# Optimization experiments

Hardware: AMD Instinct MI355X
Metric: run time of the kernel (lower is better)

The kernel has to match this reference:

```python
import jax, jax.numpy as jnp
import numpy as np

D_MODEL = 1024
N_HEADS = 16
D_K = D_MODEL // N_HEADS  # 64


def setup_inputs() -> dict:
    key = jax.random.key(0)
    ks = jax.random.split(key, 12)
    B, S = 2, 2048
    inp = {
        "query": jax.random.normal(ks[0], (B, S, D_MODEL), jnp.float32),
        "key": jax.random.normal(ks[1], (B, S, D_MODEL), jnp.float32),
        "value": jax.random.normal(ks[2], (B, S, D_MODEL), jnp.float32),
        "mask": jnp.ones((B, 1, S, S), jnp.int32),
    }
    sc = 1.0 / np.sqrt(D_MODEL)
    inp["Wq"] = jax.random.normal(ks[3], (D_MODEL, D_MODEL), jnp.float32) * sc
    inp["bq"] = jnp.zeros((D_MODEL,), jnp.float32)
    inp["Wk"] = jax.random.normal(ks[4], (D_MODEL, D_MODEL), jnp.float32) * sc
    inp["bk"] = jnp.zeros((D_MODEL,), jnp.float32)
    inp["Wv"] = jax.random.normal(ks[5], (D_MODEL, D_MODEL), jnp.float32) * sc
    inp["bv"] = jnp.zeros((D_MODEL,), jnp.float32)
    inp["Wo"] = jax.random.normal(ks[6], (D_MODEL, D_MODEL), jnp.float32) * sc
    inp["bo"] = jnp.zeros((D_MODEL,), jnp.float32)
    return inp


def reference(query, key, value, mask, Wq, bq, Wk, bk, Wv, bv, Wo, bo):
    B, Sq, _ = query.shape
    H, dk = N_HEADS, D_K
    # linear projections, split heads: (B,S,D) -> (B,H,S,dk)
    def split_heads(x):
        return x.reshape(B, -1, H, dk).transpose(0, 2, 1, 3)
    Q = split_heads(query @ Wq.T + bq)
    K = split_heads(key @ Wk.T + bk)
    V = split_heads(value @ Wv.T + bv)
    scale = 1.0 / jnp.sqrt(jnp.asarray(dk, jnp.float32))
    scores = jnp.einsum('bhqd,bhkd->bhqk', Q, K) * scale
    scores = jnp.where(mask == 0, jnp.asarray(-1e9, scores.dtype), scores)
    attn = jax.nn.softmax(scores, axis=-1)  # (B,H,Sq,Sk)
    out = jnp.einsum('bhqk,bhkd->bhqd', attn, V)
    out = out.transpose(0, 2, 1, 3).reshape(B, Sq, D_MODEL)
    out = out @ Wo.T + bo
    return out, attn
```

## Files before the change

### kernel.cpp

```cpp
#include <hip/hip_runtime.h>
#include <cstdint>
#include <cstddef>

#define DEV __device__ __forceinline__

typedef float f32x4 __attribute__((ext_vector_type(4)));
typedef __bf16 bf16x8 __attribute__((ext_vector_type(8)));
typedef unsigned short u16x8 __attribute__((ext_vector_type(8)));

static constexpr int D = 1024, H = 16, DK = 64, S = 2048, B = 2;
static constexpr int M_TOT = B * S;
static constexpr size_t OUT0 = (size_t)M_TOT * D;

DEV unsigned short f2bf(float f) {
  unsigned x = __builtin_bit_cast(unsigned, f);
  unsigned r = (x + 0x7fffu + ((x >> 16) & 1u)) >> 16;
  return (unsigned short)r;
}

DEV float bf2f(unsigned short u) {
  return __builtin_bit_cast(float, (unsigned)u << 16);
}

DEV f32x4 mfma_bf16(bf16x8 a, bf16x8 b, f32x4 c) {
  return __builtin_amdgcn_mfma_f32_16x16x32_bf16(a, b, c, 0, 0, 0);
}

DEV bf16x8 bc(u16x8 u) { return __builtin_bit_cast(bf16x8, u); }

template <int MODE, bool ABF16>
DEV void proj_body(unsigned short* As, unsigned short* Bs, const void* Aptr,
                   const unsigned short* W, const float* bias, void* dst) {
  constexpr int BM = 128, BK = 32, LDT = 40;
  const int tid = threadIdx.x;
  const int lane = tid & 63, wave = tid >> 6;
  const int wrow = wave >> 1, wcol = wave & 1;
  const int l15 = lane & 15, kg = lane >> 4;
  const int m0 = blockIdx.y * BM, n0 = blockIdx.x * BM;
  const int srow = tid >> 1, scb = (tid & 1) * 16;

  f32x4 acc[4][4] = {};

  for (int kt = 0; kt < D; kt += BK) {
    {
      u16x8 t0, t1;
      if constexpr (ABF16) {
        const unsigned short* ap =
            (const unsigned short*)Aptr + (size_t)(m0 + srow) * D + kt + scb;
        t0 = *(const u16x8*)ap;
        t1 = *(const u16x8*)(ap + 8);
      } else {
        const float* ap = (const float*)Aptr + (size_t)(m0 + srow) * D + kt + scb;
        float4 v0 = *(const float4*)(ap + 0);
        float4 v1 = *(const float4*)(ap + 4);
        float4 v2 = *(const float4*)(ap + 8);
        float4 v3 = *(const float4*)(ap + 12);
        t0[0] = f2bf(v0.x); t0[1] = f2bf(v0.y); t0[2] = f2bf(v0.z); t0[3] = f2bf(v0.w);
        t0[4] = f2bf(v1.x); t0[5] = f2bf(v1.y); t0[6] = f2bf(v1.z); t0[7] = f2bf(v1.w);
        t1[0] = f2bf(v2.x); t1[1] = f2bf(v2.y); t1[2] = f2bf(v2.z); t1[3] = f2bf(v2.w);
        t1[4] = f2bf(v3.x); t1[5] = f2bf(v3.y); t1[6] = f2bf(v3.z); t1[7] = f2bf(v3.w);
      }
      *(u16x8*)&As[srow * LDT + scb] = t0;
      *(u16x8*)&As[srow * LDT + scb + 8] = t1;

      const unsigned short* wp = W + (size_t)(n0 + srow) * D + kt + scb;
      *(u16x8*)&Bs[srow * LDT + scb] = *(const u16x8*)wp;
      *(u16x8*)&Bs[srow * LDT + scb + 8] = *(const u16x8*)(wp + 8);
    }
    __syncthreads();

    bf16x8 a[4], b[4];
#pragma unroll
    for (int i = 0; i < 4; i++)
      a[i] = bc(*(const u16x8*)&As[(wrow * 64 + i * 16 + l15) * LDT + kg * 8]);
#pragma unroll
    for (int i = 0; i < 4; i++)
      b[i] = bc(*(const u16x8*)&Bs[(wcol * 64 + i * 16 + l15) * LDT + kg * 8]);
#pragma unroll
    for (int mi = 0; mi < 4; mi++)
#pragma unroll
      for (int ni = 0; ni < 4; ni++) acc[mi][ni] = mfma_bf16(a[mi], b[ni], acc[mi][ni]);
    __syncthreads();
  }

#pragma unroll
  for (int mi = 0; mi < 4; mi++) {
#pragma unroll
    for (int ni = 0; ni < 4; ni++) {
      const int n = n0 + wcol * 64 + ni * 16 + l15;
      const float bval = bias[n];
#pragma unroll
      for (int r = 0; r < 4; r++) {
        const int m = m0 + wrow * 64 + mi * 16 + kg * 4 + r;
        float v = acc[mi][ni][r] + bval;
        if constexpr (MODE == 0) v *= 0.125f;
        if constexpr (MODE == 0 || MODE == 1) {
          const int b_ = m >> 11, s = m & (S - 1), h = n >> 6, d_ = n & (DK - 1);
          ((unsigned short*)dst)[(((size_t)(b_ * H + h)) * S + s) * DK + d_] = f2bf(v);
        } else if constexpr (MODE == 2) {
          const int b_ = m >> 11, s = m & (S - 1), h = n >> 6, d_ = n & (DK - 1);
          ((unsigned short*)dst)[(((size_t)(b_ * H + h)) * DK + d_) * S + s] = f2bf(v);
        } else {
          ((float*)dst)[(size_t)m * D + n] = v;
        }
      }
    }
  }
}

__global__ __launch_bounds__(256) void conv_kernel(
    const float* __restrict__ Wq, const float* __restrict__ Wk,
    const float* __restrict__ Wv, const float* __restrict__ Wo,
    unsigned short* __restrict__ Wqb, unsigned short* __restrict__ Wkb,
    unsigned short* __restrict__ Wvb, unsigned short* __restrict__ Wob,
    const int* __restrict__ mask, unsigned long long* __restrict__ bits) {
  const int gid = blockIdx.x, tid = threadIdx.x;
  if (gid < 256) {
    const float* srcs[4] = {Wq, Wk, Wv, Wo};
    unsigned short* dsts[4] = {Wqb, Wkb, Wvb, Wob};
    const float* src = srcs[gid >> 6];
    unsigned short* dst = dsts[gid >> 6];
    const size_t off = (size_t)(gid & 63) * 16384;
#pragma unroll
    for (int it = 0; it < 4; it++) {
      const size_t i0 = off + it * 4096 + (size_t)tid * 16;
      float4 v0 = *(const float4*)(src + i0);
      float4 v1 = *(const float4*)(src + i0 + 4);
      float4 v2 = *(const float4*)(src + i0 + 8);
      float4 v3 = *(const float4*)(src + i0 + 12);
      u16x8 t0, t1;
      t0[0] = f2bf(v0.x); t0[1] = f2bf(v0.y); t0[2] = f2bf(v0.z); t0[3] = f2bf(v0.w);
      t0[4] = f2bf(v1.x); t0[5] = f2bf(v1.y); t0[6] = f2bf(v1.z); t0[7] = f2bf(v1.w);
      t1[0] = f2bf(v2.x); t1[1] = f2bf(v2.y); t1[2] = f2bf(v2.z); t1[3] = f2bf(v2.w);
      t1[4] = f2bf(v3.x); t1[5] = f2bf(v3.y); t1[6] = f2bf(v3.z); t1[7] = f2bf(v3.w);
      *(u16x8*)(dst + i0) = t0;
      *(u16x8*)(dst + i0 + 8) = t1;
    }
  } else {
    const int lane = tid & 63;
    const int base = (gid - 256) * 256;
    for (int w = base + (tid >> 6); w < base + 256; w += 4) {
      int m = __builtin_nontemporal_load(mask + (size_t)w * 64 + lane);
      unsigned long long bal = __ballot(m != 0);
      if (lane == 0) bits[w] = bal;
    }
  }
}

struct GemmArgs {
  const float* A[3];
  const unsigned short* Wb[3];
  const float* bias[3];
  unsigned short* dst[3];
};

__global__ __launch_bounds__(256) void qkv_gemm(GemmArgs ga) {
  __shared__ __align__(16) unsigned short As[128 * 40];
  __shared__ __align__(16) unsigned short Bs[128 * 40];
  const int z = blockIdx.z;
  if (z == 0)
    proj_body<0, false>(As, Bs, ga.A[0], ga.Wb[0], ga.bias[0], ga.dst[0]);
  else if (z == 1)
    proj_body<1, false>(As, Bs, ga.A[1], ga.Wb[1], ga.bias[1], ga.dst[1]);
  else
    proj_body<2, false>(As, Bs, ga.A[2], ga.Wb[2], ga.bias[2], ga.dst[2]);
}

__global__ __launch_bounds__(256) void out_proj(const unsigned short* __restrict__ ctx,
                                                const unsigned short* __restrict__ Wob,
                                                const float* __restrict__ bo,
                                                float* __restrict__ out) {
  __shared__ __align__(16) unsigned short As[128 * 40];
  __shared__ __align__(16) unsigned short Bs[128 * 40];
  proj_body<3, true>(As, Bs, ctx, Wob, bo, out);
}

__global__ __launch_bounds__(512, 6) void attn_kernel(
    const unsigned short* __restrict__ Qb, const unsigned short* __restrict__ Kb,
    const unsigned short* __restrict__ Vt, const unsigned* __restrict__ bits32,
    float* __restrict__ attn_out, unsigned short* __restrict__ ctx) {
  constexpr int QB = 32;
  constexpr int PROW = 264;
  __shared__ __align__(16) unsigned short pbuf[2][QB * PROW];
  __shared__ unsigned mlds[QB * 64];
  __shared__ float rsum[8 * QB];
  __shared__ float rinv_s[QB];
  __shared__ float opart[4 * QB * 17];
  __shared__ unsigned mflag;

  const int wg = blockIdx.x;
  const int qblk = wg & 63, h = (wg >> 6) & 15, b_ = wg >> 10;
  const int bh = b_ * H + h;
  const int qb0 = qblk * QB;
  const int tid = threadIdx.x, lane = tid & 63, wave = tid >> 6;
  const int l15 = lane & 15, kg = lane >> 4;
  const int rowq = kg * 4;
  constexpr float LOG2E = 1.44269504088896340736f;

  if (tid == 0) mflag = 0xFFFFFFFFu;
  unsigned myand = 0xFFFFFFFFu;
  unsigned mw[4];
#pragma unroll
  for (int i = 0; i < 4; i++) {
    const int idx = tid + i * 512;
    mw[i] = bits32[((size_t)b_ * S + qb0 + (idx >> 6)) * 64 + (idx & 63)];
    myand &= mw[i];
  }
  __syncthreads();
#pragma unroll
  for (int i = 0; i < 4; i++) mlds[tid + i * 512] = mw[i];
  if (myand != 0xFFFFFFFFu) atomicAnd(&mflag, 0u);

  const unsigned short* qbase = Qb + ((size_t)bh * S + qb0) * DK;
  bf16x8 aq[2][2];
#pragma unroll
  for (int rg = 0; rg < 2; rg++)
#pragma unroll
    for (int hf = 0; hf < 2; hf++)
      aq[rg][hf] =
          bc(*(const u16x8*)(qbase + (size_t)(rg * 16 + l15) * DK + hf * 32 + kg * 8));
  __syncthreads();
  const bool allones = (mflag == 0xFFFFFFFFu);

  float sum[2][4] = {};
#pragma unroll 2
  for (int i = 0; i < 16; i++) {
    const int t = wave * 16 + i;
    const unsigned short* krow = Kb + ((size_t)bh * S + t * 16 + l15) * DK;
    bf16x8 b0 = bc(*(const u16x8*)(krow + kg * 8));
    bf16x8 b1 = bc(*(const u16x8*)(krow + 32 + kg * 8));
    const unsigned shift = (unsigned)((t & 1) * 16 + l15);
#pragma unroll
    for (int rg = 0; rg < 2; rg++) {
      f32x4 c = {0.f, 0.f, 0.f, 0.f};
      c = mfma_bf16(aq[rg][0], b0, c);
      c = mfma_bf16(aq[rg][1], b1, c);
      if (allones) {
#pragma unroll
        for (int r = 0; r < 4; r++) sum[rg][r] += exp2f(c[r] * LOG2E);
      } else {
#pragma unroll
        for (int r = 0; r < 4; r++) {
          const unsigned w = mlds[(rg * 16 + rowq + r) * 64 + (t >> 1)];
          sum[rg][r] += ((w >> shift) & 1u) ? exp2f(c[r] * LOG2E) : 0.f;
        }
      }
    }
  }

#pragma unroll
  for (int rg = 0; rg < 2; rg++)
#pragma unroll
    for (int r = 0; r < 4; r++) {
      float s = sum[rg][r];
      s += __shfl_xor(s, 1);
      s += __shfl_xor(s, 2);
      s += __shfl_xor(s, 4);
      s += __shfl_xor(s, 8);
      if (l15 == 0) rsum[wave * QB + rg * 16 + rowq + r] = s;
    }
  __syncthreads();
  if (tid < QB) {
    float t2 = 0.f;
#pragma unroll
    for (int w = 0; w < 8; w++) t2 += rsum[w * QB + tid];
    rinv_s[tid] = 1.f / t2;
  }
  __syncthreads();

  float ri[2][4];
#pragma unroll
  for (int rg = 0; rg < 2; rg++)
#pragma unroll
    for (int r = 0; r < 4; r++) ri[rg][r] = rinv_s[rg * 16 + rowq + r];

  const int dg = wave & 3, ksub = wave >> 2;
  const unsigned short* vrow = Vt + ((size_t)bh * DK + dg * 16 + l15) * S + ksub * 128;
  float* abase = attn_out + ((size_t)bh * S + qb0) * S;
  const int wrow2 = lane >> 5;
  const int wcol = (lane & 31) * 8;
  f32x4 o[2] = {};

  for (int sb = 0; sb < 8; sb++) {
    unsigned short* pb = pbuf[sb & 1];
#pragma unroll
    for (int j = 0; j < 2; j++) {
      const int t = sb * 16 + wave * 2 + j;
      const unsigned short* krow = Kb + ((size_t)bh * S + t * 16 + l15) * DK;
      bf16x8 b0 = bc(*(const u16x8*)(krow + kg * 8));
      bf16x8 b1 = bc(*(const u16x8*)(krow + 32 + kg * 8));
      const unsigned shift = (unsigned)((t & 1) * 16 + l15);
      const int lc = (wave * 2 + j) * 16 + l15;
#pragma unroll
      for (int rg = 0; rg < 2; rg++) {
        f32x4 c = {0.f, 0.f, 0.f, 0.f};
        c = mfma_bf16(aq[rg][0], b0, c);
        c = mfma_bf16(aq[rg][1], b1, c);
        if (allones) {
#pragma unroll
          for (int r = 0; r < 4; r++) {
            const int row = rg * 16 + rowq + r;
            pb[row * PROW + lc] = f2bf(exp2f(c[r] * LOG2E) * ri[rg][r]);
          }
        } else {
#pragma unroll
          for (int r = 0; r < 4; r++) {
            const int row = rg * 16 + rowq + r;
            const unsigned w = mlds[row * 64 + (t >> 1)];
            const float e = ((w >> shift) & 1u) ? exp2f(c[r] * LOG2E) : 0.f;
            pb[row * PROW + lc] = f2bf(e * ri[rg][r]);
          }
        }
      }
    }
    __syncthreads();

#pragma unroll
    for (int rr = 0; rr < 2; rr++) {
      const int row = wave * 4 + rr * 2 + wrow2;
      u16x8 u = *(const u16x8*)&pb[row * PROW + wcol];
      f32x4 lo, hi;
      lo[0] = bf2f(u[0]); lo[1] = bf2f(u[1]); lo[2] = bf2f(u[2]); lo[3] = bf2f(u[3]);
      hi[0] = bf2f(u[4]); hi[1] = bf2f(u[5]); hi[2] = bf2f(u[6]); hi[3] = bf2f(u[7]);
      float* dp = abase + (size_t)row * S + sb * 256 + wcol;
      __builtin_nontemporal_store(lo, (f32x4*)dp);
      __builtin_nontemporal_store(hi, (f32x4*)(dp + 4));
    }

    const unsigned short* vv = vrow + sb * 256;
#pragma unroll
    for (int ks = 0; ks < 4; ks++) {
      bf16x8 bv = bc(*(const u16x8*)(vv + ks * 32 + kg * 8));
#pragma unroll
      for (int rg = 0; rg < 2; rg++) {
        bf16x8 af = bc(
            *(const u16x8*)&pb[(rg * 16 + l15) * PROW + ksub * 128 + ks * 32 + kg * 8]);
        o[rg] = mfma_bf16(af, bv, o[rg]);
      }
    }
  }

  if (ksub == 1) {
#pragma unroll
    for (int rg = 0; rg < 2; rg++)
#pragma unroll
      for (int r = 0; r < 4; r++)
        opart[dg * (QB * 17) + (rg * 16 + rowq + r) * 17 + l15] = o[rg][r];
  }
  __syncthreads();
  if (ksub == 0) {
#pragma unroll
    for (int rg = 0; rg < 2; rg++)
#pragma unroll
      for (int r = 0; r < 4; r++) {
        const int row = rg * 16 + rowq + r;
        const float v = o[rg][r] + opart[dg * (QB * 17) + row * 17 + l15];
        ctx[((size_t)(b_ * S + qb0 + row)) * D + h * DK + dg * 16 + l15] = f2bf(v);
      }
  }
}

extern "C" void kernel_launch(void* const* d_in, const int* in_sizes, int n_in,
                              void* d_out, int out_size, void* d_ws, size_t ws_size,
                              hipStream_t stream) {
  const float* query = (const float*)d_in[0];
  const float* key   = (const float*)d_in[1];
  const float* value = (const float*)d_in[2];
  const int*   mask  = (const int*)d_in[3];
  const float* Wq = (const float*)d_in[4];
  const float* bq = (const float*)d_in[5];
  const float* Wk = (const float*)d_in[6];
  const float* bk = (const float*)d_in[7];
  const float* Wv = (const float*)d_in[8];
  const float* bv = (const float*)d_in[9];
  const float* Wo = (const float*)d_in[10];
  const float* bo = (const float*)d_in[11];

  float* out_p = (float*)d_out;
  float* attn_p = (float*)d_out + OUT0;

  size_t off = 0;
  auto carve = [&](size_t bytes) {
    void* p = (char*)d_ws + off;
    off += (bytes + 255) & ~(size_t)255;
    return p;
  };
  const size_t headed = (size_t)B * H * S * DK * sizeof(unsigned short);
  const size_t wbytes = (size_t)D * D * sizeof(unsigned short);
  unsigned short* Qb = (unsigned short*)carve(headed);
  unsigned short* Kb = (unsigned short*)carve(headed);
  unsigned short* Vt = (unsigned short*)carve(headed);
  unsigned short* ctx = (unsigned short*)carve((size_t)M_TOT * D * sizeof(unsigned short));
  unsigned long long* bits = (unsigned long long*)carve((size_t)B * S * S / 8);
  unsigned short* Wqb = (unsigned short*)carve(wbytes);
  unsigned short* Wkb = (unsigned short*)carve(wbytes);
  unsigned short* Wvb = (unsigned short*)carve(wbytes);
  unsigned short* Wob = (unsigned short*)carve(wbytes);

  conv_kernel<<<768, 256, 0, stream>>>(Wq, Wk, Wv, Wo, Wqb, Wkb, Wvb, Wob, mask, bits);

  GemmArgs ga;
  ga.A[0] = query; ga.A[1] = key; ga.A[2] = value;
  ga.Wb[0] = Wqb; ga.Wb[1] = Wkb; ga.Wb[2] = Wvb;
  ga.bias[0] = bq; ga.bias[1] = bk; ga.bias[2] = bv;
  ga.dst[0] = Qb; ga.dst[1] = Kb; ga.dst[2] = Vt;
  qkv_gemm<<<dim3(8, 32, 3), 256, 0, stream>>>(ga);

  attn_kernel<<<B * H * (S / 32), 512, 0, stream>>>(Qb, Kb, Vt, (const unsigned*)bits,
                                                    attn_p, ctx);

  out_proj<<<dim3(8, 32), 256, 0, stream>>>(ctx, Wob, bo, out_p);
}
```

Baseline: 369.5 us.

## Trim attention LDS, raise occupancy, and defer attn-probability stores by one stage

Removes the shared-memory copy of the mask bits; the mask is now read straight from global memory, and the check for an all-ones mask uses a simple flag. The output-partial scratch buffer now reuses the P double buffer instead of its own allocation, and the launch-bounds occupancy hint goes from 6 to 8. The fp32 attention-matrix store for each block is moved to the start of the next iteration (plus a final flush), so the global writes overlap the next QK/exp compute. The aim is to hide the large attention-output write stream and fit more resident workgroups per CU. The cost is possible register spilling under the tighter bound and slower global mask reads on the masked path.

```diff
diff --git a/kernel.cpp b/kernel.cpp
--- a/kernel.cpp
+++ b/kernel.cpp
@@ -175,17 +175,15 @@
   proj_body<3, true>(As, Bs, ctx, Wob, bo, out);
 }
 
-__global__ __launch_bounds__(512, 6) void attn_kernel(
+__global__ __launch_bounds__(512, 8) void attn_kernel(
     const unsigned short* __restrict__ Qb, const unsigned short* __restrict__ Kb,
     const unsigned short* __restrict__ Vt, const unsigned* __restrict__ bits32,
     float* __restrict__ attn_out, unsigned short* __restrict__ ctx) {
   constexpr int QB = 32;
   constexpr int PROW = 264;
   __shared__ __align__(16) unsigned short pbuf[2][QB * PROW];
-  __shared__ unsigned mlds[QB * 64];
   __shared__ float rsum[8 * QB];
   __shared__ float rinv_s[QB];
-  __shared__ float opart[4 * QB * 17];
   __shared__ unsigned mflag;
 
   const int wg = blockIdx.x;
@@ -197,19 +195,17 @@
   const int rowq = kg * 4;
   constexpr float LOG2E = 1.44269504088896340736f;
 
-  if (tid == 0) mflag = 0xFFFFFFFFu;
-  unsigned myand = 0xFFFFFFFFu;
-  unsigned mw[4];
-#pragma unroll
-  for (int i = 0; i < 4; i++) {
-    const int idx = tid + i * 512;
-    mw[i] = bits32[((size_t)b_ * S + qb0 + (idx >> 6)) * 64 + (idx & 63)];
-    myand &= mw[i];
-  }
+  const unsigned* mrow = bits32 + ((size_t)b_ * S + qb0) * 64;
+
+  if (tid == 0) mflag = 1u;
   __syncthreads();
-#pragma unroll
-  for (int i = 0; i < 4; i++) mlds[tid + i * 512] = mw[i];
-  if (myand != 0xFFFFFFFFu) atomicAnd(&mflag, 0u);
+  {
+    unsigned ok = 1u;
+#pragma unroll
+    for (int i = 0; i < 4; i++)
+      ok &= (mrow[tid + i * 512] == 0xFFFFFFFFu) ? 1u : 0u;
+    if (!ok) atomicAnd(&mflag, 0u);
+  }
 
   const unsigned short* qbase = Qb + ((size_t)bh * S + qb0) * DK;
   bf16x8 aq[2][2];
@@ -220,7 +216,7 @@
       aq[rg][hf] =
           bc(*(const u16x8*)(qbase + (size_t)(rg * 16 + l15) * DK + hf * 32 + kg * 8));
   __syncthreads();
-  const bool allones = (mflag == 0xFFFFFFFFu);
+  const bool allones = (mflag != 0u);
 
   float sum[2][4] = {};
 #pragma unroll 2
@@ -241,7 +237,7 @@
       } else {
 #pragma unroll
         for (int r = 0; r < 4; r++) {
-          const unsigned w = mlds[(rg * 16 + rowq + r) * 64 + (t >> 1)];
+          const unsigned w = mrow[(rg * 16 + rowq + r) * 64 + (t >> 1)];
           sum[rg][r] += ((w >> shift) & 1u) ? exp2f(c[r] * LOG2E) : 0.f;
         }
       }
@@ -281,7 +277,24 @@
   const int wcol = (lane & 31) * 8;
   f32x4 o[2] = {};
 
+  auto writeDuty = [&](int sbw) {
+    const unsigned short* pb = pbuf[sbw & 1];
+#pragma unroll
+    for (int rr = 0; rr < 2; rr++) {
+      const int row = wave * 4 + rr * 2 + wrow2;
+      u16x8 u = *(const u16x8*)&pb[row * PROW + wcol];
+      f32x4 lo, hi;
+      lo[0] = bf2f(u[0]); lo[1] = bf2f(u[1]); lo[2] = bf2f(u[2]); lo[3] = bf2f(u[3]);
+      hi[0] = bf2f(u[4]); hi[1] = bf2f(u[5]); hi[2] = bf2f(u[6]); hi[3] = bf2f(u[7]);
+      float* dp = abase + (size_t)row * S + sbw * 256 + wcol;
+      __builtin_nontemporal_store(lo, (f32x4*)dp);
+      __builtin_nontemporal_store(hi, (f32x4*)(dp + 4));
+    }
+  };
+
   for (int sb = 0; sb < 8; sb++) {
+    if (sb) writeDuty(sb - 1);
+
     unsigned short* pb = pbuf[sb & 1];
 #pragma unroll
     for (int j = 0; j < 2; j++) {
@@ -306,7 +319,7 @@
 #pragma unroll
           for (int r = 0; r < 4; r++) {
             const int row = rg * 16 + rowq + r;
-            const unsigned w = mlds[row * 64 + (t >> 1)];
+            const unsigned w = mrow[row * 64 + (t >> 1)];
             const float e = ((w >> shift) & 1u) ? exp2f(c[r] * LOG2E) : 0.f;
             pb[row * PROW + lc] = f2bf(e * ri[rg][r]);
           }
@@ -315,18 +328,6 @@
     }
     __syncthreads();
 
-#pragma unroll
-    for (int rr = 0; rr < 2; rr++) {
-      const int row = wave * 4 + rr * 2 + wrow2;
-      u16x8 u = *(const u16x8*)&pb[row * PROW + wcol];
-      f32x4 lo, hi;
-      lo[0] = bf2f(u[0]); lo[1] = bf2f(u[1]); lo[2] = bf2f(u[2]); lo[3] = bf2f(u[3]);
-      hi[0] = bf2f(u[4]); hi[1] = bf2f(u[5]); hi[2] = bf2f(u[6]); hi[3] = bf2f(u[7]);
-      float* dp = abase + (size_t)row * S + sb * 256 + wcol;
-      __builtin_nontemporal_store(lo, (f32x4*)dp);
-      __builtin_nontemporal_store(hi, (f32x4*)(dp + 4));
-    }
-
     const unsigned short* vv = vrow + sb * 256;
 #pragma unroll
     for (int ks = 0; ks < 4; ks++) {
@@ -339,7 +340,9 @@
       }
     }
   }
-
+  writeDuty(7);
+
+  float* opart = (float*)&pbuf[0][0];
   if (ksub == 1) {
 #pragma unroll
     for (int rg = 0; rg < 2; rg++)
```

After: 815.4 us. 121% more time.
